# Performance work log

Measured on AMD Instinct MI355X. Metric: run time of the kernel, lower is better.

## Reference

```python
import jax, jax.numpy as jnp
import numpy as np

# Constants from module-level env defaults
CONST_VAL = 10.0                       # VLLM_SOFTMAX_CONST_VAL
EPS = 1.1754943508222875e-38           # torch.finfo(torch.bfloat16).tiny
SCALE = 0.08838834764831845            # 1/sqrt(head_size=128)

B, QH, KVH, D = 32, 32, 8, 128         # batch, q heads, kv heads, head dim
NUM_CACHE_BLOCKS, BLOCK_SIZE = 600, 128
BLOCKS_PER_SEQ = 16                    # context 2048 / block_size 128
NB = B * BLOCKS_PER_SEQ                # 512 active blocks


def setup_inputs() -> dict:
    key = jax.random.key(0)
    ks = jax.random.split(key, 6)
    query = jax.random.normal(ks[0], (B, QH, D), dtype=jnp.float32)
    key_cache = jax.random.normal(ks[1], (NUM_CACHE_BLOCKS, BLOCK_SIZE, KVH, D), dtype=jnp.float32)
    value_cache = jax.random.normal(ks[2], (NUM_CACHE_BLOCKS, BLOCK_SIZE, KVH, D), dtype=jnp.float32)
    # each active block points at a distinct physical cache block
    block_list = jax.random.permutation(ks[3], NUM_CACHE_BLOCKS)[:NB].astype(jnp.int32)
    # block i belongs to sequence i // BLOCKS_PER_SEQ -> one-hot [NB, B]
    block_to_batch = jnp.arange(NB) // BLOCKS_PER_SEQ
    block_mapping = jax.nn.one_hot(block_to_batch, B, dtype=jnp.float32)
    # ALiBi-like per-position bias within each block (non-positive)
    block_bias = -5.0 * jax.random.uniform(ks[4], (NB, BLOCK_SIZE), dtype=jnp.float32)
    return {
        'query': query,
        'key_cache': key_cache,
        'value_cache': value_cache,
        'block_mapping': block_mapping,
        'block_bias': block_bias,
        'block_list': block_list,
    }


def reference(query, key_cache, value_cache, block_mapping, block_bias, block_list):
    """flat_pa decode path with the pa() const-norm softmax normalization (GQA)."""
    b, qh, d = query.shape
    kvh = key_cache.shape[2]
    g = qh // kvh                                   # queries per kv head
    nb, bs = block_bias.shape
    # batch2block(scale * query): [NB,B] @ [B, QH, D] -> [NB, QH, D]
    q = jnp.einsum('nb,bhd->nhd', block_mapping, SCALE * query)
    q = q.reshape(nb, kvh, g, 1, d)                 # [NB, KVH, G, 1, D]
    k = key_cache[block_list]                       # [NB, BS, KVH, D]
    v = value_cache[block_list]                     # [NB, BS, KVH, D]
    # attn = q @ k^T + block_bias : [NB, KVH, G, 1, BS]
    attn = jnp.einsum('nkgqd,nskd->nkgqs', q, k)
    attn = attn + block_bias[:, None, None, None, :]
    # const-norm exp (no running max; subtract fixed const)
    attn = jnp.exp(attn - CONST_VAL)
    block_sum = attn.sum(axis=-1, keepdims=True)    # [NB, KVH, G, 1, 1]
    # block2batch then batch2block: per-sequence sum broadcast back to blocks
    group_sums = jnp.einsum('nb,nkgqo->bkgqo', block_mapping, block_sum)
    group_sums = jnp.einsum('nb,bkgqo->nkgqo', block_mapping, group_sums) + EPS
    group_sums = jnp.maximum(block_sum, group_sums)
    attn = attn / group_sums
    out = jnp.einsum('nkgqs,nskd->nkgqd', attn, v)  # [NB, KVH, G, 1, D]
    # block2batch: accumulate per-block partial outputs into per-sequence output
    out = jnp.einsum('nb,nkgqd->bkgqd', block_mapping, out)
    return out.reshape(b, qh, d)                    # squeeze q-dim, flatten heads
```

## Files before the change

kernel.cpp:

```cpp
#include <hip/hip_runtime.h>

#define NBATCH 32
#define QH 32
#define KVH 8
#define G 4
#define DH 128
#define BS 128
#define NB 512
#define CONST_VAL 10.0f
#define EPS_T 1.1754943508222875e-38f
#define SCALE_F 0.08838834764831845f


__global__ void pa_zero_S(float* S) {
    int i = blockIdx.x * 256 + threadIdx.x;
    if (i < NBATCH * KVH * G) S[i] = 0.f;
}

__global__ __launch_bounds__(256) void pa_pass1(
    const float* __restrict__ query,
    const float* __restrict__ key_cache,
    const float* __restrict__ value_cache,
    const float* __restrict__ mapping,
    const float* __restrict__ bias,
    const int*   __restrict__ block_list,
    float* __restrict__ partial,
    float* __restrict__ bsum,
    float* __restrict__ S)
{
    const int n  = blockIdx.x;
    const int kh = blockIdx.y;
    const int t  = threadIdx.x;

    __shared__ float sQ[G][DH];
    __shared__ float sKV[64][129];
    __shared__ float sE[G][BS];
    __shared__ float sBs[G];

    {
        int i0 = t, i1 = t + 256;
        int g0 = i0 >> 7, d0 = i0 & 127;
        int g1 = i1 >> 7, d1 = i1 & 127;
        float qa = 0.f, qb = 0.f;
        for (int b = 0; b < NBATCH; ++b) {
            float w = mapping[n * NBATCH + b];
            if (w != 0.f) {
                const float* qrow = query + ((size_t)b * QH + (size_t)kh * G) * DH;
                qa += w * qrow[g0 * DH + d0];
                qb += w * qrow[g1 * DH + d1];
            }
        }
        sQ[g0][d0] = qa * SCALE_F;
        sQ[g1][d1] = qb * SCALE_F;
    }

    const int p = block_list[n];
    const float* kbase = key_cache   + (size_t)p * BS * KVH * DH + (size_t)kh * DH;
    const float* vbase = value_cache + (size_t)p * BS * KVH * DH + (size_t)kh * DH;
    const int row_stride = KVH * DH;

    const int s_l = t & 63;
    const int g_s = t >> 6;
    for (int ph = 0; ph < 2; ++ph) {
        __syncthreads();
        for (int i = 0; i < 8; ++i) {
            int j = i * 256 + t;
            int row = j >> 5;
            int c4  = j & 31;
            float4 kv = *(const float4*)(kbase + (size_t)(ph * 64 + row) * row_stride + c4 * 4);
            float* dst = &sKV[row][c4 * 4];
            dst[0] = kv.x; dst[1] = kv.y; dst[2] = kv.z; dst[3] = kv.w;
        }
        __syncthreads();
        float acc = 0.f;
        #pragma unroll 8
        for (int d = 0; d < DH; ++d) acc += sKV[s_l][d] * sQ[g_s][d];
        int s = ph * 64 + s_l;
        sE[g_s][s] = __expf(acc + bias[(size_t)n * BS + s] - CONST_VAL);
    }
    __syncthreads();

    {
        int wave = t >> 6, lane = t & 63;
        float v = sE[wave][lane] + sE[wave][lane + 64];
        for (int off = 32; off > 0; off >>= 1) v += __shfl_down(v, off);
        if (lane == 0) sBs[wave] = v;
    }
    __syncthreads();
    if (t < G) {
        float bsv = sBs[t];
        bsum[((size_t)n * KVH + kh) * G + t] = bsv;
        for (int b = 0; b < NBATCH; ++b) {
            float w = mapping[n * NBATCH + b];
            if (w != 0.f) atomicAdd(&S[(b * KVH + kh) * G + t], w * bsv);
        }
    }

    const int d_v = t & 127;
    const int gg  = t >> 7;
    float o0 = 0.f, o1 = 0.f;
    for (int ph = 0; ph < 2; ++ph) {
        __syncthreads();
        for (int i = 0; i < 8; ++i) {
            int j = i * 256 + t;
            int row = j >> 5;
            int c4  = j & 31;
            float4 vv = *(const float4*)(vbase + (size_t)(ph * 64 + row) * row_stride + c4 * 4);
            float* dst = &sKV[row][c4 * 4];
            dst[0] = vv.x; dst[1] = vv.y; dst[2] = vv.z; dst[3] = vv.w;
        }
        __syncthreads();
        int g0 = gg * 2, g1 = gg * 2 + 1;
        #pragma unroll 8
        for (int sl = 0; sl < 64; ++sl) {
            float v = sKV[sl][d_v];
            int s = ph * 64 + sl;
            o0 += sE[g0][s] * v;
            o1 += sE[g1][s] * v;
        }
    }
    size_t pb = (((size_t)n * KVH + kh) * G) * DH;
    partial[pb + (size_t)(gg * 2)     * DH + d_v] = o0;
    partial[pb + (size_t)(gg * 2 + 1) * DH + d_v] = o1;
}

__global__ __launch_bounds__(128) void pa_pass2(
    const float* __restrict__ mapping,
    const float* __restrict__ partial,
    const float* __restrict__ bsum,
    const float* __restrict__ S,
    float* __restrict__ out)
{
    int b  = blockIdx.x;
    int kh = blockIdx.y;
    int g  = blockIdx.z;
    int d  = threadIdx.x;
    float acc = 0.f;
    for (int n = 0; n < NB; ++n) {
        float w = mapping[n * NBATCH + b];
        if (w == 0.f) continue;
        float gs = 0.f;
        for (int bb = 0; bb < NBATCH; ++bb) {
            float w2 = mapping[n * NBATCH + bb];
            if (w2 != 0.f) gs += w2 * S[(bb * KVH + kh) * G + g];
        }
        gs += EPS_T;
        float bs = bsum[((size_t)n * KVH + kh) * G + g];
        float den = fmaxf(bs, gs);
        acc += w * partial[(((size_t)n * KVH + kh) * G + g) * DH + d] / den;
    }
    out[((size_t)b * QH + (size_t)kh * G + g) * DH + d] = acc;
}

extern "C" void kernel_launch(void* const* d_in, const int* in_sizes, int n_in,
                              void* d_out, int out_size, void* d_ws, size_t ws_size,
                              hipStream_t stream) {
    const float* query       = (const float*)d_in[0];
    const float* key_cache   = (const float*)d_in[1];
    const float* value_cache = (const float*)d_in[2];
    const float* mapping     = (const float*)d_in[3];
    const float* bias        = (const float*)d_in[4];
    const int*   block_list  = (const int*)d_in[5];
    float* out = (float*)d_out;

    float* partial = (float*)d_ws;
    float* bsum    = partial + (size_t)NB * KVH * G * DH;
    float* S       = bsum + (size_t)NB * KVH * G;

    pa_zero_S<<<4, 256, 0, stream>>>(S);
    pa_pass1<<<dim3(NB, KVH), 256, 0, stream>>>(
        query, key_cache, value_cache, mapping, bias, block_list, partial, bsum, S);
    pa_pass2<<<dim3(NBATCH, KVH, G), 128, 0, stream>>>(mapping, partial, bsum, S, out);
}
```

Before: 741.3 us.

## Precompute per-block denominators and cache mapping weights in shared memory

Adds a separate kernel that computes each block's softmax denominator once, replacing the nested 32-wide loop that pass2 ran for every (n, batch) pair. Pass2 now stages the mapping column in shared memory and each thread handles two heads, and pass1 caches the mapping row in shared memory. The aim is to remove the redundant global reads and recomputation in pass2, which scans all 512 blocks per output. The cost is an extra kernel launch and a small denominator buffer in workspace.

```diff
diff --git a/kernel.cpp b/kernel.cpp
--- a/kernel.cpp
+++ b/kernel.cpp
@@ -32,10 +32,14 @@
     const int kh = blockIdx.y;
     const int t  = threadIdx.x;
 
+    __shared__ float sW[NBATCH];
     __shared__ float sQ[G][DH];
     __shared__ float sKV[64][129];
     __shared__ float sE[G][BS];
     __shared__ float sBs[G];
+
+    if (t < NBATCH) sW[t] = mapping[n * NBATCH + t];
+    __syncthreads();
 
     {
         int i0 = t, i1 = t + 256;
@@ -43,7 +47,7 @@
         int g1 = i1 >> 7, d1 = i1 & 127;
         float qa = 0.f, qb = 0.f;
         for (int b = 0; b < NBATCH; ++b) {
-            float w = mapping[n * NBATCH + b];
+            float w = sW[b];
             if (w != 0.f) {
                 const float* qrow = query + ((size_t)b * QH + (size_t)kh * G) * DH;
                 qa += w * qrow[g0 * DH + d0];
@@ -91,7 +95,7 @@
         float bsv = sBs[t];
         bsum[((size_t)n * KVH + kh) * G + t] = bsv;
         for (int b = 0; b < NBATCH; ++b) {
-            float w = mapping[n * NBATCH + b];
+            float w = sW[b];
             if (w != 0.f) atomicAdd(&S[(b * KVH + kh) * G + t], w * bsv);
         }
     }
@@ -124,32 +128,52 @@
     partial[pb + (size_t)(gg * 2 + 1) * DH + d_v] = o1;
 }
 
-__global__ __launch_bounds__(128) void pa_pass2(
+__global__ __launch_bounds__(256) void pa_den(
+    const float* __restrict__ mapping,
+    const float* __restrict__ bsum,
+    const float* __restrict__ S,
+    float* __restrict__ den)
+{
+    int i = blockIdx.x * 256 + threadIdx.x;
+    if (i >= NB * KVH * G) return;
+    int g  = i & (G - 1);
+    int kh = (i / G) & (KVH - 1);
+    int n  = i / (G * KVH);
+    float gs = 0.f;
+    for (int b = 0; b < NBATCH; ++b)
+        gs += mapping[n * NBATCH + b] * S[(b * KVH + kh) * G + g];
+    gs += EPS_T;
+    den[i] = fmaxf(bsum[i], gs);
+}
+
+__global__ __launch_bounds__(256) void pa_pass2(
     const float* __restrict__ mapping,
     const float* __restrict__ partial,
-    const float* __restrict__ bsum,
-    const float* __restrict__ S,
+    const float* __restrict__ den,
     float* __restrict__ out)
 {
     int b  = blockIdx.x;
     int kh = blockIdx.y;
-    int g  = blockIdx.z;
-    int d  = threadIdx.x;
-    float acc = 0.f;
+    int t  = threadIdx.x;
+    int g  = t >> 7;
+    int d  = t & 127;
+
+    __shared__ float sWc[NB];
+    for (int i = t; i < NB; i += 256) sWc[i] = mapping[i * NBATCH + b];
+    __syncthreads();
+
+    float a0 = 0.f, a1 = 0.f;
     for (int n = 0; n < NB; ++n) {
-        float w = mapping[n * NBATCH + b];
+        float w = sWc[n];
         if (w == 0.f) continue;
-        float gs = 0.f;
-        for (int bb = 0; bb < NBATCH; ++bb) {
-            float w2 = mapping[n * NBATCH + bb];
-            if (w2 != 0.f) gs += w2 * S[(bb * KVH + kh) * G + g];
-        }
-        gs += EPS_T;
-        float bs = bsum[((size_t)n * KVH + kh) * G + g];
-        float den = fmaxf(bs, gs);
-        acc += w * partial[(((size_t)n * KVH + kh) * G + g) * DH + d] / den;
-    }
-    out[((size_t)b * QH + (size_t)kh * G + g) * DH + d] = acc;
+        int di = (n * KVH + kh) * G;
+        size_t pb = (size_t)di * DH;
+        a0 += w * partial[pb + (size_t)g * DH + d] / den[di + g];
+        a1 += w * partial[pb + (size_t)(g + 2) * DH + d] / den[di + g + 2];
+    }
+    size_t ob = ((size_t)b * QH + (size_t)kh * G) * DH;
+    out[ob + (size_t)g * DH + d]       = a0;
+    out[ob + (size_t)(g + 2) * DH + d] = a1;
 }
 
 extern "C" void kernel_launch(void* const* d_in, const int* in_sizes, int n_in,
@@ -166,9 +190,11 @@
     float* partial = (float*)d_ws;
     float* bsum    = partial + (size_t)NB * KVH * G * DH;
     float* S       = bsum + (size_t)NB * KVH * G;
+    float* den     = S + (size_t)NBATCH * KVH * G;
 
     pa_zero_S<<<4, 256, 0, stream>>>(S);
     pa_pass1<<<dim3(NB, KVH), 256, 0, stream>>>(
         query, key_cache, value_cache, mapping, bias, block_list, partial, bsum, S);
-    pa_pass2<<<dim3(NBATCH, KVH, G), 128, 0, stream>>>(mapping, partial, bsum, S, out);
-}
+    pa_den<<<(NB * KVH * G + 255) / 256, 256, 0, stream>>>(mapping, bsum, S, den);
+    pa_pass2<<<dim3(NBATCH, KVH), 256, 0, stream>>>(mapping, partial, den, out);
+}
```

New measurement: 642.1 us. 13.4% less time.
